# Performance work log

Hardware: AMD Instinct MI355X
Metric: run time of the kernel (lower is better)

Reference implementation:

```python
import jax, jax.numpy as jnp
import numpy as np

EPS = 1e-08
KERNEL = 3


def setup_inputs() -> dict:
    key = jax.random.key(0)
    k1, k2, k3, k4 = jax.random.split(key, 4)
    N, IN_CH, OUT_CH, H, W, STYLE_DIM = 16, 256, 256, 64, 64, 512
    x = jax.random.normal(k1, (N, IN_CH, H, W), dtype=jnp.float32)
    style = jax.random.normal(k2, (N, STYLE_DIM), dtype=jnp.float32)
    # base weight: [1, out_ch, in_ch, k, k] (torch.randn init)
    weight = jax.random.normal(k3, (1, OUT_CH, IN_CH, KERNEL, KERNEL), dtype=jnp.float32)
    # modulation Linear(style_dim -> in_ch): weight ~ N(0,1), bias = 0
    mod_w = jax.random.normal(k4, (IN_CH, STYLE_DIM), dtype=jnp.float32)
    mod_b = jnp.zeros((IN_CH,), dtype=jnp.float32)
    return {"x": x, "style": style, "weight": weight, "mod_w": mod_w, "mod_b": mod_b}


def _per_sample_conv(xi, wi):
    # xi: [in_ch, H, W], wi: [out_ch, in_ch, k, k]
    pad = KERNEL // 2
    out = jax.lax.conv_general_dilated(
        xi[None], wi,
        window_strides=(1, 1),
        padding=[(pad, pad), (pad, pad)],
        dimension_numbers=("NCHW", "OIHW", "NCHW"),
    )
    return out[0]  # [out_ch, H, W]


def reference(x, style, weight, mod_w, mod_b):
    # modulation: Linear(style) -> [N, in_ch]
    s = style @ mod_w.T + mod_b  # [N, in_ch]
    # modulate base weight: [N, out_ch, in_ch, k, k]
    w = weight * (s[:, None, :, None, None] + 1.0)
    # demodulate
    demod = jax.lax.rsqrt(jnp.sum(w * w, axis=(2, 3, 4)) + EPS)  # [N, out_ch]
    w = w * demod[:, :, None, None, None]
    # grouped conv with groups=N == per-sample conv, vmapped over batch
    out = jax.vmap(_per_sample_conv)(x, w)  # [N, out_ch, H, W]
    return out
```

## Files before the change

kernel.cpp:

```cpp
#include <hip/hip_runtime.h>
#include <hip/hip_bf16.h>
#include <stdint.h>


#define NB  16
#define IC  256
#define OC  256
#define HW  64
#define HWP 66
#define SD  512
#define SPATIAL 4096

typedef __hip_bfloat16 bf16;
typedef __bf16 bf16x8 __attribute__((ext_vector_type(8)));
typedef float  f32x4  __attribute__((ext_vector_type(4)));
typedef uint32_t u32a3 __attribute__((address_space(3)));
typedef const uint32_t u32a1 __attribute__((address_space(1)));

static __device__ __forceinline__ unsigned short f2bu(float f) {
    bf16 h = __float2bfloat16(f);
    union { bf16 b; unsigned short u; } c; c.b = h; return c.u;
}
static __device__ __forceinline__ void gll16(const void* g, void* l) {
    __builtin_amdgcn_global_load_lds((u32a1*)g, (u32a3*)l, 16, 0, 0);
}

__global__ __launch_bounds__(256)
void k_prep1(const float* __restrict__ weight, const float* __restrict__ style,
             const float* __restrict__ mod_w, const float* __restrict__ mod_b,
             float* __restrict__ wsq, bf16* __restrict__ wt2,
             uint4* __restrict__ xs4, float* __restrict__ scale) {
    int b = blockIdx.x, t = threadIdx.x;
    if (b < 256) {
        int tid = b * 256 + t;
        const float* wp = weight + (size_t)tid * 9;
        float v[9], s = 0.f;
        #pragma unroll
        for (int r = 0; r < 9; ++r) { v[r] = wp[r]; s += v[r] * v[r]; }
        wsq[tid] = s;
        #pragma unroll
        for (int r = 0; r < 9; ++r) wt2[(r << 16) + tid] = __float2bfloat16(v[r]);
    } else if (b < 784) {
        int idx = b - 256;
        int n = idx / 33, bx = idx - n * 33;
        int f = bx * 256 + t;
        int u = f >> 5, q = f & 31;
        if (u >= 260) return;
        int rb;
        if      (u <  66) rb = u;
        else if (u < 132) rb = 65 * 66 + (u - 66);
        else if (u < 196) rb = (u - 131) * 66;
        else              rb = (u - 195) * 66 + 65;
        xs4[(size_t)n * 139392 + rb * 32 + q] = make_uint4(0u, 0u, 0u, 0u);
    } else {
        int lane = t & 63;
        int w = (b - 784) * 4 + (t >> 6);
        int n = w >> 8, ic = w & 255;
        const float4* mw4 = (const float4*)mod_w + (size_t)ic * 128 + lane * 2;
        const float4* st4 = (const float4*)style + (size_t)n * 128 + lane * 2;
        float4 a0 = mw4[0], a1 = mw4[1], s0 = st4[0], s1 = st4[1];
        float acc = a0.x*s0.x + a0.y*s0.y + a0.z*s0.z + a0.w*s0.w
                  + a1.x*s1.x + a1.y*s1.y + a1.z*s1.z + a1.w*s1.w;
        #pragma unroll
        for (int off = 32; off > 0; off >>= 1) acc += __shfl_down(acc, off);
        if (lane == 0) scale[w] = acc + mod_b[ic] + 1.0f;
    }
}

__global__ __launch_bounds__(256)
void k_prep2(const float* __restrict__ x, const float* __restrict__ scale,
             const float* __restrict__ wsq, bf16* __restrict__ xs,
             float* __restrict__ demod) {
    __shared__ unsigned short tile[HW * 264];
    int b = blockIdx.x, t = threadIdx.x;
    if (b < 1024) {
        int y = b & 63, n = b >> 6;
        const float* sc = scale + n * IC;
        const float4* xp4 = (const float4*)(x + ((size_t)n * IC) * SPATIAL + (size_t)y * HW);
        #pragma unroll
        for (int i = 0; i < 16; ++i) {
            int fid = i * 256 + t;
            int ic = fid >> 4, f4 = fid & 15;
            float4 v = xp4[(size_t)ic * 1024 + f4];
            float s = sc[ic];
            int sp = f4 * 4;
            tile[(sp + 0) * 264 + ic] = f2bu(v.x * s);
            tile[(sp + 1) * 264 + ic] = f2bu(v.y * s);
            tile[(sp + 2) * 264 + ic] = f2bu(v.z * s);
            tile[(sp + 3) * 264 + ic] = f2bu(v.w * s);
        }
        __syncthreads();
        uint4* dst4 = (uint4*)(xs + (((size_t)n * HWP + (y + 1)) * HWP + 1) * IC);
        #pragma unroll
        for (int j = 0; j < 8; ++j) {
            int uid = j * 256 + t;
            int sp = uid >> 5, g = uid & 31;
            dst4[sp * 32 + g] = *(const uint4*)&tile[sp * 264 + g * 8];
        }
    } else {
        int n = b - 1024, oc = t;
        float* sc = (float*)tile;
        sc[t] = scale[n * IC + t];
        __syncthreads();
        const float4* wp4 = (const float4*)(wsq + (size_t)oc * IC);
        const float4* sc4 = (const float4*)sc;
        float acc = 0.f;
        #pragma unroll 8
        for (int i = 0; i < 64; ++i) {
            float4 q = wp4[i], s = sc4[i];
            acc += q.x*s.x*s.x + q.y*s.y*s.y + q.z*s.z*s.z + q.w*s.w*s.w;
        }
        demod[n * OC + oc] = rsqrtf(acc + 1e-8f);
    }
}

__global__ __launch_bounds__(256, 4)
void k_conv(const bf16* __restrict__ xs, const bf16* __restrict__ wt2,
            const float* __restrict__ demod, float* __restrict__ out) {
    __shared__ unsigned short Al[128 * 64];
    __shared__ unsigned short Bl[128 * 64];
    int t = threadIdx.x, l = t & 63, w = t >> 6;
    int wm = w & 1, wn = w >> 1;
    int bid = blockIdx.x;
    int work = ((bid & 7) << 7) | (bid >> 3);
    int bn = work & 1, st = work >> 1;
    int n = st >> 5;
    int sp_base = (st & 31) << 7;
    int oc_base = bn << 7;

    int lrow = l >> 3;
    int lseg = (l & 7) ^ lrow;
    int sp0 = sp_base + w * 32 + lrow;
    const bf16* gA0 = xs + (((size_t)n * HWP + (sp0 >> 6)) * HWP + (sp0 & 63)) * IC + lseg * 8;
    const bf16* gB0 = wt2 + (size_t)(oc_base + w * 32 + lrow) * IC + lseg * 8;
    char* Ab = (char*)Al + w * 4096;
    char* Bb = (char*)Bl + w * 4096;

    f32x4 acc[4][4];
    #pragma unroll
    for (int i = 0; i < 4; ++i)
        #pragma unroll
        for (int j = 0; j < 4; ++j) acc[i][j] = (f32x4){0.f, 0.f, 0.f, 0.f};

    int rAbase = (wm * 64 + (l & 15)) * 64;
    int rBbase = (wn * 64 + (l & 15)) * 64;
    int q0 = l >> 4, xk = l & 7;

    for (int ch = 0; ch < 36; ++ch) {
        int r = ch >> 2;
        int ic0 = (ch & 3) << 6;
        int ky = r / 3, kx = r - ky * 3;
        int aoff = (ky * HWP + kx) * IC + ic0;
        int boff = (r << 16) + ic0;
        __syncthreads();
        #pragma unroll
        for (int i = 0; i < 4; ++i)
            gll16(gA0 + aoff + i * 2048, Ab + i * 1024);
        #pragma unroll
        for (int i = 0; i < 4; ++i)
            gll16(gB0 + boff + i * 2048, Bb + i * 1024);
        __syncthreads();
        #pragma unroll
        for (int kk = 0; kk < 2; ++kk) {
            int ks = (((kk << 2) + q0) ^ xk) << 3;
            bf16x8 af[4], bfr[4];
            #pragma unroll
            for (int mi = 0; mi < 4; ++mi)
                af[mi] = *reinterpret_cast<const bf16x8*>(&Al[rAbase + mi * 1024 + ks]);
            #pragma unroll
            for (int ni = 0; ni < 4; ++ni)
                bfr[ni] = *reinterpret_cast<const bf16x8*>(&Bl[rBbase + ni * 1024 + ks]);
            #pragma unroll
            for (int mi = 0; mi < 4; ++mi)
                #pragma unroll
                for (int ni = 0; ni < 4; ++ni)
                    acc[mi][ni] = __builtin_amdgcn_mfma_f32_16x16x32_bf16(
                        af[mi], bfr[ni], acc[mi][ni], 0, 0, 0);
        }
    }

    const float* dm = demod + n * OC;
    int ocol = l & 15, orow = (l >> 4) << 2;
    #pragma unroll
    for (int ni = 0; ni < 4; ++ni) {
        int oc = oc_base + wn * 64 + ni * 16 + ocol;
        float d = dm[oc];
        size_t ob = ((size_t)(n * OC + oc)) * SPATIAL + sp_base + wm * 64 + orow;
        #pragma unroll
        for (int mi = 0; mi < 4; ++mi) {
            f32x4 a = acc[mi][ni];
            f32x4 o = { a[0] * d, a[1] * d, a[2] * d, a[3] * d };
            *reinterpret_cast<f32x4*>(out + ob + mi * 16) = o;
        }
    }
}

extern "C" void kernel_launch(void* const* d_in, const int* in_sizes, int n_in,
                              void* d_out, int out_size, void* d_ws, size_t ws_size,
                              hipStream_t stream) {
    const float* x      = (const float*)d_in[0];
    const float* style  = (const float*)d_in[1];
    const float* weight = (const float*)d_in[2];
    const float* mod_w  = (const float*)d_in[3];
    const float* mod_b  = (const float*)d_in[4];
    float* out = (float*)d_out;

    char* ws = (char*)d_ws;
    float* scale = (float*)(ws + 0);
    float* demod = (float*)(ws + 16384);
    float* wsq   = (float*)(ws + 32768);
    bf16*  wt2   = (bf16*)(ws + 294912);
    bf16*  xs    = (bf16*)(ws + 1474560);

    k_prep1<<<1808, 256, 0, stream>>>(weight, style, mod_w, mod_b,
                                      wsq, wt2, (uint4*)xs, scale);
    k_prep2<<<1040, 256, 0, stream>>>(x, scale, wsq, xs, demod);
    k_conv<<<1024, 256, 0, stream>>>(xs, wt2, demod, out);
}
```

Before: 202.0 us.

## Fuse input modulation, bf16 packing and demod into conv kernel with LDS halo tile

Removes the separate prep2 pass that scaled x, converted it to padded channel-last bf16 in a global workspace, and computed demod. The conv kernel now loads fp32 x directly per 64-channel chunk, applies the style scale, packs it into a swizzled LDS tile covering two output rows plus halo, and reuses that tile across all 9 taps. Demod is computed per block in the prologue. Blocks grow to 512 threads covering all 256 output channels. This cuts the global round trip of the intermediate activation and one launch, in exchange for redundant demod work per block, a heavier block and scattered fp32 loads inside the main loop.

```diff
diff --git a/kernel.cpp b/kernel.cpp
--- a/kernel.cpp
+++ b/kernel.cpp
@@ -7,7 +7,6 @@
 #define IC  256
 #define OC  256
 #define HW  64
-#define HWP 66
 #define SD  512
 #define SPATIAL 4096
 
@@ -29,7 +28,7 @@
 void k_prep1(const float* __restrict__ weight, const float* __restrict__ style,
              const float* __restrict__ mod_w, const float* __restrict__ mod_b,
              float* __restrict__ wsq, bf16* __restrict__ wt2,
-             uint4* __restrict__ xs4, float* __restrict__ scale) {
+             float* __restrict__ scale) {
     int b = blockIdx.x, t = threadIdx.x;
     if (b < 256) {
         int tid = b * 256 + t;
@@ -40,21 +39,9 @@
         wsq[tid] = s;
         #pragma unroll
         for (int r = 0; r < 9; ++r) wt2[(r << 16) + tid] = __float2bfloat16(v[r]);
-    } else if (b < 784) {
-        int idx = b - 256;
-        int n = idx / 33, bx = idx - n * 33;
-        int f = bx * 256 + t;
-        int u = f >> 5, q = f & 31;
-        if (u >= 260) return;
-        int rb;
-        if      (u <  66) rb = u;
-        else if (u < 132) rb = 65 * 66 + (u - 66);
-        else if (u < 196) rb = (u - 131) * 66;
-        else              rb = (u - 195) * 66 + 65;
-        xs4[(size_t)n * 139392 + rb * 32 + q] = make_uint4(0u, 0u, 0u, 0u);
     } else {
         int lane = t & 63;
-        int w = (b - 784) * 4 + (t >> 6);
+        int w = (b - 256) * 4 + (t >> 6);
         int n = w >> 8, ic = w & 255;
         const float4* mw4 = (const float4*)mod_w + (size_t)ic * 128 + lane * 2;
         const float4* st4 = (const float4*)style + (size_t)n * 128 + lane * 2;
@@ -67,74 +54,43 @@
     }
 }
 
-__global__ __launch_bounds__(256)
-void k_prep2(const float* __restrict__ x, const float* __restrict__ scale,
-             const float* __restrict__ wsq, bf16* __restrict__ xs,
-             float* __restrict__ demod) {
-    __shared__ unsigned short tile[HW * 264];
-    int b = blockIdx.x, t = threadIdx.x;
-    if (b < 1024) {
-        int y = b & 63, n = b >> 6;
-        const float* sc = scale + n * IC;
-        const float4* xp4 = (const float4*)(x + ((size_t)n * IC) * SPATIAL + (size_t)y * HW);
-        #pragma unroll
-        for (int i = 0; i < 16; ++i) {
-            int fid = i * 256 + t;
-            int ic = fid >> 4, f4 = fid & 15;
-            float4 v = xp4[(size_t)ic * 1024 + f4];
-            float s = sc[ic];
-            int sp = f4 * 4;
-            tile[(sp + 0) * 264 + ic] = f2bu(v.x * s);
-            tile[(sp + 1) * 264 + ic] = f2bu(v.y * s);
-            tile[(sp + 2) * 264 + ic] = f2bu(v.z * s);
-            tile[(sp + 3) * 264 + ic] = f2bu(v.w * s);
-        }
-        __syncthreads();
-        uint4* dst4 = (uint4*)(xs + (((size_t)n * HWP + (y + 1)) * HWP + 1) * IC);
-        #pragma unroll
-        for (int j = 0; j < 8; ++j) {
-            int uid = j * 256 + t;
-            int sp = uid >> 5, g = uid & 31;
-            dst4[sp * 32 + g] = *(const uint4*)&tile[sp * 264 + g * 8];
-        }
-    } else {
-        int n = b - 1024, oc = t;
-        float* sc = (float*)tile;
-        sc[t] = scale[n * IC + t];
-        __syncthreads();
-        const float4* wp4 = (const float4*)(wsq + (size_t)oc * IC);
-        const float4* sc4 = (const float4*)sc;
-        float acc = 0.f;
-        #pragma unroll 8
-        for (int i = 0; i < 64; ++i) {
-            float4 q = wp4[i], s = sc4[i];
-            acc += q.x*s.x*s.x + q.y*s.y*s.y + q.z*s.z*s.z + q.w*s.w*s.w;
-        }
-        demod[n * OC + oc] = rsqrtf(acc + 1e-8f);
-    }
-}
+__global__ __launch_bounds__(512, 4)
+void k_conv(const float* __restrict__ x, const bf16* __restrict__ wt2,
+            const float* __restrict__ scale, const float* __restrict__ wsq,
+            float* __restrict__ out) {
+    __shared__ uint32_t As[4 * 66 * 32];
+    __shared__ uint32_t Bs[256 * 32];
+    __shared__ float sc_s[256];
+    __shared__ float dm_s[256];
 
-__global__ __launch_bounds__(256, 4)
-void k_conv(const bf16* __restrict__ xs, const bf16* __restrict__ wt2,
-            const float* __restrict__ demod, float* __restrict__ out) {
-    __shared__ unsigned short Al[128 * 64];
-    __shared__ unsigned short Bl[128 * 64];
     int t = threadIdx.x, l = t & 63, w = t >> 6;
     int wm = w & 1, wn = w >> 1;
     int bid = blockIdx.x;
-    int work = ((bid & 7) << 7) | (bid >> 3);
-    int bn = work & 1, st = work >> 1;
-    int n = st >> 5;
-    int sp_base = (st & 31) << 7;
-    int oc_base = bn << 7;
+    int work = ((bid & 7) << 6) | (bid >> 3);
+    int n = work >> 5, st = work & 31;
+    int y0 = st << 1;
+    int sp_base = st << 7;
 
-    int lrow = l >> 3;
-    int lseg = (l & 7) ^ lrow;
-    int sp0 = sp_base + w * 32 + lrow;
-    const bf16* gA0 = xs + (((size_t)n * HWP + (sp0 >> 6)) * HWP + (sp0 & 63)) * IC + lseg * 8;
-    const bf16* gB0 = wt2 + (size_t)(oc_base + w * 32 + lrow) * IC + lseg * 8;
-    char* Ab = (char*)Al + w * 4096;
-    char* Bb = (char*)Bl + w * 4096;
+    if (t < 256) {
+        sc_s[t] = scale[n * IC + t];
+        const float4* wq4 = (const float4*)(wsq + (size_t)t * IC);
+        const float4* sl4 = (const float4*)(scale + (size_t)n * IC);
+        float acc = 0.f;
+        #pragma unroll 4
+        for (int i = 0; i < 64; ++i) {
+            float4 q = wq4[i], s = sl4[i];
+            acc += q.x*s.x*s.x + q.y*s.y*s.y + q.z*s.z*s.z + q.w*s.w*s.w;
+        }
+        dm_s[t] = rsqrtf(acc + 1e-8f);
+        int ypz = t >> 6, cz = (t >> 5) & 1, icpz = t & 31;
+        int xz = cz ? 65 : 0;
+        int segp = (icpz >> 2) ^ (((xz >> 2) ^ xz) & 7);
+        As[(ypz * 66 + xz) * 32 + segp * 4 + (icpz & 3)] = 0u;
+    }
+
+    int lrow = l >> 3, lseg = (l & 7) ^ lrow;
+    const bf16* gB0 = wt2 + (size_t)(w * 32 + lrow) * IC + lseg * 8;
+    char* Bb = (char*)Bs + w * 4096;
 
     f32x4 acc[4][4];
     #pragma unroll
@@ -142,49 +98,75 @@
         #pragma unroll
         for (int j = 0; j < 4; ++j) acc[i][j] = (f32x4){0.f, 0.f, 0.f, 0.f};
 
-    int rAbase = (wm * 64 + (l & 15)) * 64;
-    int rBbase = (wn * 64 + (l & 15)) * 64;
-    int q0 = l >> 4, xk = l & 7;
+    int q0 = l >> 4, l15 = l & 15, l7 = l & 7;
+    const float4* x4 = (const float4*)x;
 
-    for (int ch = 0; ch < 36; ++ch) {
-        int r = ch >> 2;
-        int ic0 = (ch & 3) << 6;
-        int ky = r / 3, kx = r - ky * 3;
-        int aoff = (ky * HWP + kx) * IC + ic0;
-        int boff = (r << 16) + ic0;
+    for (int c = 0; c < 4; ++c) {
+        int ic0 = c << 6;
         __syncthreads();
         #pragma unroll
-        for (int i = 0; i < 4; ++i)
-            gll16(gA0 + aoff + i * 2048, Ab + i * 1024);
-        #pragma unroll
-        for (int i = 0; i < 4; ++i)
-            gll16(gB0 + boff + i * 2048, Bb + i * 1024);
-        __syncthreads();
-        #pragma unroll
-        for (int kk = 0; kk < 2; ++kk) {
-            int ks = (((kk << 2) + q0) ^ xk) << 3;
-            bf16x8 af[4], bfr[4];
+        for (int j = 0; j < 4; ++j) {
+            int u = j * 512 + t;
+            int xq = u & 15, yp = (u >> 4) & 3, icp = u >> 6;
+            int ic = ic0 + (icp << 1);
+            int y = y0 + yp - 1;
+            int vok = ((unsigned)y < 64u) ? 1 : 0;
+            size_t bx = ((size_t)((n * IC + ic) * 64 + (vok ? y : 0))) * 16 + xq;
+            float4 va = x4[bx], vb = x4[bx + 1024];
+            float sa = vok ? sc_s[ic] : 0.f;
+            float sb = vok ? sc_s[ic + 1] : 0.f;
+            float av[4] = {va.x, va.y, va.z, va.w};
+            float bv[4] = {vb.x, vb.y, vb.z, vb.w};
+            int xb = (xq << 2) + 1;
             #pragma unroll
-            for (int mi = 0; mi < 4; ++mi)
-                af[mi] = *reinterpret_cast<const bf16x8*>(&Al[rAbase + mi * 1024 + ks]);
+            for (int e = 0; e < 4; ++e) {
+                int xc = xb + e;
+                int segp = (icp >> 2) ^ (((xc >> 2) ^ xc) & 7);
+                As[(yp * 66 + xc) * 32 + segp * 4 + (icp & 3)] =
+                    (uint32_t)f2bu(av[e] * sa) | ((uint32_t)f2bu(bv[e] * sb) << 16);
+            }
+        }
+        for (int r = 0; r < 9; ++r) {
+            int ky = r / 3, kx = r - ky * 3;
+            int boff = (r << 16) + ic0;
+            __syncthreads();
             #pragma unroll
-            for (int ni = 0; ni < 4; ++ni)
-                bfr[ni] = *reinterpret_cast<const bf16x8*>(&Bl[rBbase + ni * 1024 + ks]);
+            for (int i = 0; i < 4; ++i)
+                gll16(gB0 + boff + i * 2048, Bb + i * 1024);
+            __syncthreads();
             #pragma unroll
-            for (int mi = 0; mi < 4; ++mi)
+            for (int kk = 0; kk < 2; ++kk) {
+                int g = (kk << 2) + q0;
+                bf16x8 af[4], bfr[4];
                 #pragma unroll
-                for (int ni = 0; ni < 4; ++ni)
-                    acc[mi][ni] = __builtin_amdgcn_mfma_f32_16x16x32_bf16(
-                        af[mi], bfr[ni], acc[mi][ni], 0, 0, 0);
+                for (int mi = 0; mi < 4; ++mi) {
+                    int col = mi * 16 + l15 + kx;
+                    int pos = (wm + ky) * 66 + col;
+                    int segp = g ^ (((col >> 2) ^ col) & 7);
+                    af[mi] = *reinterpret_cast<const bf16x8*>(
+                        (const unsigned short*)As + pos * 64 + segp * 8);
+                }
+                #pragma unroll
+                for (int ni = 0; ni < 4; ++ni) {
+                    int rB = wn * 64 + ni * 16 + l15;
+                    bfr[ni] = *reinterpret_cast<const bf16x8*>(
+                        (const unsigned short*)Bs + rB * 64 + ((g ^ l7) << 3));
+                }
+                #pragma unroll
+                for (int mi = 0; mi < 4; ++mi)
+                    #pragma unroll
+                    for (int ni = 0; ni < 4; ++ni)
+                        acc[mi][ni] = __builtin_amdgcn_mfma_f32_16x16x32_bf16(
+                            af[mi], bfr[ni], acc[mi][ni], 0, 0, 0);
+            }
         }
     }
 
-    const float* dm = demod + n * OC;
-    int ocol = l & 15, orow = (l >> 4) << 2;
+    int orow = (l >> 4) << 2;
     #pragma unroll
     for (int ni = 0; ni < 4; ++ni) {
-        int oc = oc_base + wn * 64 + ni * 16 + ocol;
-        float d = dm[oc];
+        int oc = wn * 64 + ni * 16 + l15;
+        float d = dm_s[oc];
         size_t ob = ((size_t)(n * OC + oc)) * SPATIAL + sp_base + wm * 64 + orow;
         #pragma unroll
         for (int mi = 0; mi < 4; ++mi) {
@@ -207,13 +189,9 @@
 
     char* ws = (char*)d_ws;
     float* scale = (float*)(ws + 0);
-    float* demod = (float*)(ws + 16384);
-    float* wsq   = (float*)(ws + 32768);
-    bf16*  wt2   = (bf16*)(ws + 294912);
-    bf16*  xs    = (bf16*)(ws + 1474560);
+    float* wsq   = (float*)(ws + 16384);
+    bf16*  wt2   = (bf16*)(ws + 278528);
 
-    k_prep1<<<1808, 256, 0, stream>>>(weight, style, mod_w, mod_b,
-                                      wsq, wt2, (uint4*)xs, scale);
-    k_prep2<<<1040, 256, 0, stream>>>(x, scale, wsq, xs, demod);
-    k_conv<<<1024, 256, 0, stream>>>(xs, wt2, demod, out);
+    k_prep1<<<1280, 256, 0, stream>>>(weight, style, mod_w, mod_b, wsq, wt2, scale);
+    k_conv<<<512, 512, 0, stream>>>(x, wt2, scale, wsq, out);
 }
```

Result: slower. 241.6 us (+19.6%).
